# Kernel tuning notes

Measured on AMD Instinct MI355X. Metric: run time of the kernel, lower is better.

Reference implementation:

```python
import jax, jax.numpy as jnp
import numpy as np
from jax import lax

N_FFT = 1024
HOP = 64
SR = 16000
N_MELS = 80
N_ITER = 300
N_FRAMES = 512
N_BINS = N_FFT // 2 + 1  # 513
SIG_LEN = N_FFT + HOP * (N_FRAMES - 1)  # 33728 (center=False istft length)

# periodic hann window (librosa default, sym=False)
_WIN_NP = (0.5 - 0.5 * np.cos(2.0 * np.pi * np.arange(N_FFT) / N_FFT)).astype(np.float32)
_WIN = jnp.asarray(_WIN_NP)
# frame gather indices for center=False framing: [N_FRAMES, N_FFT]
_FRAME_IDX_NP = np.arange(N_FRAMES)[:, None] * HOP + np.arange(N_FFT)[None, :]
_FRAME_IDX = jnp.asarray(_FRAME_IDX_NP)
# window-sum-squares normalization for istft overlap-add
_wss = np.zeros(SIG_LEN, np.float32)
np.add.at(_wss, _FRAME_IDX_NP, np.broadcast_to(_WIN_NP**2, (N_FRAMES, N_FFT)))
_WSS_SAFE = jnp.asarray(np.where(_wss > 1e-11, _wss, 1.0).astype(np.float32))


def _mel_filterbank(sr, n_fft, n_mels, fmin=0.0, fmax=None):
    """librosa.filters.mel with defaults: slaney mel scale, slaney norm."""
    if fmax is None:
        fmax = sr / 2.0
    f_sp = 200.0 / 3.0
    min_log_hz = 1000.0
    min_log_mel = min_log_hz / f_sp
    logstep = np.log(6.4) / 27.0

    def hz2mel(f):
        f = np.asarray(f, dtype=np.float64)
        return np.where(f >= min_log_hz,
                        min_log_mel + np.log(np.maximum(f, min_log_hz) / min_log_hz) / logstep,
                        f / f_sp)

    def mel2hz(m):
        m = np.asarray(m, dtype=np.float64)
        return np.where(m >= min_log_mel,
                        min_log_hz * np.exp(logstep * (m - min_log_mel)),
                        m * f_sp)

    mel_f = mel2hz(np.linspace(hz2mel(fmin), hz2mel(fmax), n_mels + 2))
    fft_f = np.linspace(0.0, sr / 2.0, 1 + n_fft // 2)
    fdiff = np.diff(mel_f)
    ramps = mel_f[:, None] - fft_f[None, :]
    lower = -ramps[:-2] / fdiff[:-1, None]
    upper = ramps[2:] / fdiff[1:, None]
    weights = np.maximum(0.0, np.minimum(lower, upper))
    enorm = 2.0 / (mel_f[2:n_mels + 2] - mel_f[:n_mels])  # slaney norm
    weights *= enorm[:, None]
    return weights.astype(np.float32)  # [n_mels, n_bins]


def _stft(x):
    # x: [SIG_LEN] -> [N_BINS, N_FRAMES], center=False, hann window
    frames = x[_FRAME_IDX] * _WIN  # [N_FRAMES, N_FFT]
    return jnp.fft.rfft(frames, axis=-1).T


def _istft(S):
    # S: [N_BINS, N_FRAMES] -> [SIG_LEN], center=False, hann window, NOLA norm
    frames = jnp.fft.irfft(S.T, n=N_FFT, axis=-1) * _WIN  # [N_FRAMES, N_FFT]
    ola = jnp.zeros(SIG_LEN, dtype=frames.dtype).at[_FRAME_IDX].add(frames)
    return ola / _WSS_SAFE


def setup_inputs() -> dict:
    key = jax.random.key(0)
    mel = jax.random.normal(key, (N_MELS, N_FRAMES), dtype=jnp.float32)
    basis = _mel_filterbank(SR, N_FFT, N_MELS)           # [80, 513]
    inv_mel_basis = np.linalg.pinv(basis).astype(np.float32)  # [513, 80]
    return {"mel": mel, "inv_mel_basis": jnp.asarray(inv_mel_basis)}


def reference(mel, inv_mel_basis):
    # mel -> linear magnitude via pseudo-inverse mel basis
    mag = inv_mel_basis @ jnp.power(10.0, mel)  # [N_BINS, N_FRAMES]

    def step(X_best, _):
        x_t = _istft(X_best)
        est = _stft(x_t)
        phase = est / jnp.maximum(1e-8, jnp.abs(est))
        return (mag * phase).astype(jnp.complex64), None

    X0 = mag.astype(jnp.complex64)
    X_final, _ = lax.scan(step, X0, None, length=N_ITER)
    return jnp.real(_istft(X_final))  # [SIG_LEN]
```

## Files before the change

kernel.cpp:

```cpp
#include <hip/hip_runtime.h>
#include <math.h>

#define NFFT   1024
#define NH     512
#define HOP    64
#define NMELS  80
#define NFR    512
#define NBINS  513
#define NITER  300
#define SIGLEN 33728
#define NSEG   527
#define NT     256
#define NB     512

#define TBL_WIN  0
#define TBL_TWR  1024
#define TBL_TWI  1280
#define TBL_W1R  1536
#define TBL_W1I  2056
#define OFF_MAG  4096
#define OFF_IWS  266752
#define OFF_F    300480
#define OFF_F2   824768
#define FGEN     1349056

typedef unsigned long long u64;
typedef unsigned int u32;

__device__ __forceinline__ float4 coh_load4(const float* p) {
    u64 a = __hip_atomic_load((const u64*)p,       __ATOMIC_RELAXED, __HIP_MEMORY_SCOPE_AGENT);
    u64 b = __hip_atomic_load((const u64*)(p + 2), __ATOMIC_RELAXED, __HIP_MEMORY_SCOPE_AGENT);
    float2 fa, fb;
    __builtin_memcpy(&fa, &a, 8);
    __builtin_memcpy(&fb, &b, 8);
    return make_float4(fa.x, fa.y, fb.x, fb.y);
}
__device__ __forceinline__ void coh_store4(float* p, float4 v) {
    float2 fa = make_float2(v.x, v.y), fb = make_float2(v.z, v.w);
    u64 a, b;
    __builtin_memcpy(&a, &fa, 8);
    __builtin_memcpy(&b, &fb, 8);
    __hip_atomic_store((u64*)p,       a, __ATOMIC_RELAXED, __HIP_MEMORY_SCOPE_AGENT);
    __hip_atomic_store((u64*)(p + 2), b, __ATOMIC_RELAXED, __HIP_MEMORY_SCOPE_AGENT);
}
__device__ __forceinline__ float coh_load1(const float* p) {
    u32 a = __hip_atomic_load((const u32*)p, __ATOMIC_RELAXED, __HIP_MEMORY_SCOPE_AGENT);
    float f;
    __builtin_memcpy(&f, &a, 4);
    return f;
}
__device__ __forceinline__ void flag_store(int* p, int v) {
    __hip_atomic_store(p, v, __ATOMIC_RELAXED, __HIP_MEMORY_SCOPE_AGENT);
}
__device__ __forceinline__ int flag_load(const int* p) {
    return __hip_atomic_load(p, __ATOMIC_RELAXED, __HIP_MEMORY_SCOPE_AGENT);
}
__device__ __forceinline__ float4 f4add(float4 a, float4 b) {
    return make_float4(a.x + b.x, a.y + b.y, a.z + b.z, a.w + b.w);
}

template<int P, int SH, bool INV>
__device__ __forceinline__ void r4b(const float* __restrict__ sR, const float* __restrict__ sI,
                                    float* __restrict__ dR, float* __restrict__ dI,
                                    const float* twr, const float* twi, int j) {
    int k  = j & (P - 1);
    int d0 = ((j - k) << 2) + k;
    float x0r = sR[j],       x0i = sI[j];
    float x1r = sR[j + 128], x1i = sI[j + 128];
    float x2r = sR[j + 256], x2i = sI[j + 256];
    float x3r = sR[j + 384], x3i = sI[j + 384];
    int tb = k << SH;
    float c1 = twr[tb], s1 = twi[tb];
    if (INV) s1 = -s1;
    float c2 = c1 * c1 - s1 * s1, s2 = 2.f * c1 * s1;
    float c3 = c1 * c2 - s1 * s2, s3 = c1 * s2 + s1 * c2;
    float a1r = x1r * c1 - x1i * s1, a1i = x1r * s1 + x1i * c1;
    float a2r = x2r * c2 - x2i * s2, a2i = x2r * s2 + x2i * c2;
    float a3r = x3r * c3 - x3i * s3, a3i = x3r * s3 + x3i * c3;
    float t0r = x0r + a2r, t0i = x0i + a2i;
    float t1r = x0r - a2r, t1i = x0i - a2i;
    float t2r = a1r + a3r, t2i = a1i + a3i;
    float t3r = a1r - a3r, t3i = a1i - a3i;
    float i3r = INV ? -t3i : t3i;
    float i3i = INV ?  t3r : -t3r;
    dR[d0]         = t0r + t2r;  dI[d0]         = t0i + t2i;
    dR[d0 + P]     = t1r + i3r;  dI[d0 + P]     = t1i + i3i;
    dR[d0 + 2 * P] = t0r - t2r;  dI[d0 + 2 * P] = t0i - t2i;
    dR[d0 + 3 * P] = t1r - i3r;  dI[d0 + 3 * P] = t1i - i3i;
}

struct __align__(16) SMemI {
    float xb[NFFT];
    float C0r[NH], C0i[NH];
    float C1r[NH], C1i[NH];
    float win[NFFT];
    float twr[256], twi[256];
    float mag[516];
};

extern "C" __global__ __launch_bounds__(NT)
void k_init(const float* __restrict__ mel,
            const float* __restrict__ invmel,
            float* __restrict__ ws) {
    __shared__ SMemI sm;
    const int tid = threadIdx.x;
    const int t   = blockIdx.x;

    for (int n = tid; n < NFFT; n += NT) {
        double a = (2.0 * 3.14159265358979323846) * (double)n / 1024.0;
        sm.win[n] = (float)(0.5 - 0.5 * cos(a));
    }
    for (int j = tid; j < 256; j += NT) {
        double a = (2.0 * 3.14159265358979323846) * (double)j / 512.0;
        sm.twr[j] = (float)cos(a);
        sm.twi[j] = (float)(-sin(a));
    }
    __syncthreads();
    if (t == 0) {
        for (int n = tid; n < NFFT; n += NT) ws[TBL_WIN + n] = sm.win[n];
        for (int j = tid; j < 256; j += NT) {
            ws[TBL_TWR + j] = sm.twr[j];
            ws[TBL_TWI + j] = sm.twi[j];
        }
        for (int k = tid; k < NBINS; k += NT) {
            double a = (2.0 * 3.14159265358979323846) * (double)k / 1024.0;
            ws[TBL_W1R + k] = (float)cos(a);
            ws[TBL_W1I + k] = (float)sin(a);
        }
        for (int i = tid; i < NFR * 16; i += NT)
            ((int*)ws)[FGEN + i] = 0;
    }

    for (int p = t * NT + tid; p < SIGLEN; p += NFR * NT) {
        int tq = p >> 6, io = p & 63;
        float s = 0.f;
#pragma unroll
        for (int m = 0; m < 16; ++m) {
            int tp = tq - m;
            if (tp >= 0 && tp < NFR) {
                float w = sm.win[io + (m << 6)];
                s += w * w;
            }
        }
        ws[OFF_IWS + p] = (s > 1e-11f) ? (1.0f / s) : 1.0f;
    }

    if (tid < NMELS) sm.xb[tid] = exp10f(mel[tid * NFR + t]);
    __syncthreads();
    for (int k = tid; k < NBINS; k += NT) {
        const float* row = invmel + k * NMELS;
        float s = 0.f;
#pragma unroll 8
        for (int j = 0; j < NMELS; ++j) s += row[j] * sm.xb[j];
        ws[OFF_MAG + t * NBINS + k] = s;
        sm.mag[k] = s;
    }
    __syncthreads();

    for (int k = tid; k < NH; k += NT) {
        float xr = sm.mag[k], yr = sm.mag[512 - k];
        double a = (2.0 * 3.14159265358979323846) * (double)k / 1024.0;
        float c = (float)cos(a), s = (float)sin(a);
        float dr = xr - yr;
        sm.C1r[k] = ((xr + yr) - s * dr) * (1.0f / 1024.0f);
        sm.C1i[k] = (c * dr) * (1.0f / 1024.0f);
    }
    __syncthreads();
    if (tid < 128) {
        float x0r = sm.C1r[tid],       x0i = sm.C1i[tid];
        float x1r = sm.C1r[tid + 128], x1i = sm.C1i[tid + 128];
        float x2r = sm.C1r[tid + 256], x2i = sm.C1i[tid + 256];
        float x3r = sm.C1r[tid + 384], x3i = sm.C1i[tid + 384];
        float t0r = x0r + x2r, t0i = x0i + x2i;
        float t1r = x0r - x2r, t1i = x0i - x2i;
        float t2r = x1r + x3r, t2i = x1i + x3i;
        float t3r = x1r - x3r, t3i = x1i - x3i;
        float4 vr = make_float4(t0r + t2r, t1r - t3i, t0r - t2r, t1r + t3i);
        float4 vi = make_float4(t0i + t2i, t1i + t3r, t0i - t2i, t1i - t3r);
        ((float4*)sm.C0r)[tid] = vr;
        ((float4*)sm.C0i)[tid] = vi;
    }
    __syncthreads();
    if (tid < 128) r4b<4, 5, true>(sm.C0r, sm.C0i, sm.C1r, sm.C1i, sm.twr, sm.twi, tid);
    __syncthreads();
    if (tid < 128) r4b<16, 3, true>(sm.C1r, sm.C1i, sm.C0r, sm.C0i, sm.twr, sm.twi, tid);
    __syncthreads();
    if (tid < 128) r4b<64, 1, true>(sm.C0r, sm.C0i, sm.C1r, sm.C1i, sm.twr, sm.twi, tid);
    __syncthreads();
    {
        float c = sm.twr[tid], s = -sm.twi[tid];
        float x0r = sm.C1r[tid], x0i = sm.C1i[tid];
        float x1r = sm.C1r[tid + 256], x1i = sm.C1i[tid + 256];
        float ar = x1r * c - x1i * s, ai = x1r * s + x1i * c;
        sm.C0r[tid]       = x0r + ar;  sm.C0i[tid]       = x0i + ai;
        sm.C0r[tid + 256] = x0r - ar;  sm.C0i[tid + 256] = x0i - ai;
    }
    __syncthreads();

    float4 w4 = ((float4*)sm.win)[tid];
    float4 o;
    o.x = w4.x * sm.C0r[2 * tid];
    o.y = w4.y * sm.C0i[2 * tid];
    o.z = w4.z * sm.C0r[2 * tid + 1];
    o.w = w4.w * sm.C0i[2 * tid + 1];
    *(float4*)&ws[OFF_F + (t << 10) + (tid << 2)] = o;
}


struct __align__(16) SM1 {
    float C0r[NH], C0i[NH];
    float C1r[NH], C1i[NH];
    float twr[256], twi[256];
};

extern "C" __global__ __launch_bounds__(NT)
void k_persist(float* __restrict__ ws, float* __restrict__ out) {
    __shared__ SM1 sm;
    const int tid = threadIdx.x;
    const int t   = blockIdx.x;
    const int i0  = tid << 2;
    const int j2  = 512 - tid;
    const int n0  = tid << 1;

    const float* tbl  = ws;
    const float* magg = ws + OFF_MAG;
    const float* iws  = ws + OFF_IWS;
    float* F0 = ws + OFF_F;
    float* F1 = ws + OFF_F2;
    int*   fgen = (int*)ws + FGEN;

    if (tid < 64)       ((float4*)sm.twr)[tid]      = ((const float4*)(tbl + TBL_TWR))[tid];
    else if (tid < 128) ((float4*)sm.twi)[tid - 64] = ((const float4*)(tbl + TBL_TWI))[tid - 64];

    float4 w4   = ((const float4*)(tbl + TBL_WIN))[tid];
    float4 iws4 = *(const float4*)&iws[(t << 6) + i0];
    float m_a, m_b, m_ny = 0.f, w1r_a, w1i_a, w1r_b, w1i_b;
    {
        const int s0 = t * NBINS;
        if (tid == 0) {
            m_a = magg[s0]; m_ny = magg[s0 + 512]; m_b = magg[s0 + 256];
            w1r_a = 1.f; w1i_a = 0.f; w1r_b = 0.f; w1i_b = 1.f;
        } else {
            m_a = magg[s0 + tid]; m_b = magg[s0 + j2];
            w1r_a = tbl[TBL_W1R + tid]; w1i_a = tbl[TBL_W1I + tid];
            w1r_b = tbl[TBL_W1R + j2];  w1i_b = tbl[TBL_W1I + j2];
        }
    }
    const bool extra = (t >= 497);
    int gseg = -1;
    if (tid < 64) gseg = t;
    else if (tid < 128 && extra) gseg = t + 15;
    const int u = tid & 63;
    float iwreg = 0.f;
    if (gseg >= 0) iwreg = iws[(gseg << 6) + u];

    const int q    = tid >> 4;
    const int tq   = t + q;
    const int foff = i0 & 63;
    const bool interior = (t >= 15 && t <= NFR - 16);

#pragma unroll 1
    for (int it = 1; it <= NITER; ++it) {
        if (it > 1 && tid < 31) {
            int tp = t - 15 + tid;
            if (tp >= 0 && tp < NFR) {
                const int* fp = fgen + (tp << 4);
                if (flag_load(fp) < it - 1) {
                    do { __builtin_amdgcn_s_sleep(4); } while (flag_load(fp) < it - 1);
                }
            }
        }
        __syncthreads();

        const float* Fs = (it & 1) ? F0 : F1;
        float*       Fd = (it & 1) ? F1 : F0;

        float4 acc;
        if (interior) {
            float4 v0  = coh_load4(&Fs[((tq)      << 10) + foff]);
            float4 v1  = coh_load4(&Fs[((tq - 1)  << 10) + foff + (1 << 6)]);
            float4 v2  = coh_load4(&Fs[((tq - 2)  << 10) + foff + (2 << 6)]);
            float4 v3  = coh_load4(&Fs[((tq - 3)  << 10) + foff + (3 << 6)]);
            float4 v4  = coh_load4(&Fs[((tq - 4)  << 10) + foff + (4 << 6)]);
            float4 v5  = coh_load4(&Fs[((tq - 5)  << 10) + foff + (5 << 6)]);
            float4 v6  = coh_load4(&Fs[((tq - 6)  << 10) + foff + (6 << 6)]);
            float4 v7  = coh_load4(&Fs[((tq - 7)  << 10) + foff + (7 << 6)]);
            float4 v8  = coh_load4(&Fs[((tq - 8)  << 10) + foff + (8 << 6)]);
            float4 v9  = coh_load4(&Fs[((tq - 9)  << 10) + foff + (9 << 6)]);
            float4 v10 = coh_load4(&Fs[((tq - 10) << 10) + foff + (10 << 6)]);
            float4 v11 = coh_load4(&Fs[((tq - 11) << 10) + foff + (11 << 6)]);
            float4 v12 = coh_load4(&Fs[((tq - 12) << 10) + foff + (12 << 6)]);
            float4 v13 = coh_load4(&Fs[((tq - 13) << 10) + foff + (13 << 6)]);
            float4 v14 = coh_load4(&Fs[((tq - 14) << 10) + foff + (14 << 6)]);
            float4 v15 = coh_load4(&Fs[((tq - 15) << 10) + foff + (15 << 6)]);
            float4 s0 = f4add(f4add(v0, v1),  f4add(v2, v3));
            float4 s1 = f4add(f4add(v4, v5),  f4add(v6, v7));
            float4 s2 = f4add(f4add(v8, v9),  f4add(v10, v11));
            float4 s3 = f4add(f4add(v12, v13), f4add(v14, v15));
            acc = f4add(f4add(s0, s1), f4add(s2, s3));
        } else {
            acc = make_float4(0.f, 0.f, 0.f, 0.f);
#pragma unroll
            for (int m = 0; m < 16; ++m) {
                int tp = tq - m;
                if (tp >= 0 && tp < NFR) {
                    float4 x = coh_load4(&Fs[(tp << 10) + foff + (m << 6)]);
                    acc.x += x.x; acc.y += x.y; acc.z += x.z; acc.w += x.w;
                }
            }
        }
        {
            float xx = acc.x * iws4.x;
            float xy = acc.y * iws4.y;
            float xz = acc.z * iws4.z;
            float xw = acc.w * iws4.w;
            sm.C1r[n0]     = xx * w4.x;
            sm.C1i[n0]     = xy * w4.y;
            sm.C1r[n0 + 1] = xz * w4.z;
            sm.C1i[n0 + 1] = xw * w4.w;
        }
        __syncthreads();
        if (tid < 128) {
            float x0r = sm.C1r[tid],       x0i = sm.C1i[tid];
            float x1r = sm.C1r[tid + 128], x1i = sm.C1i[tid + 128];
            float x2r = sm.C1r[tid + 256], x2i = sm.C1i[tid + 256];
            float x3r = sm.C1r[tid + 384], x3i = sm.C1i[tid + 384];
            float t0r = x0r + x2r, t0i = x0i + x2i;
            float t1r = x0r - x2r, t1i = x0i - x2i;
            float t2r = x1r + x3r, t2i = x1i + x3i;
            float t3r = x1r - x3r, t3i = x1i - x3i;
            float4 vr = make_float4(t0r + t2r, t1r + t3i, t0r - t2r, t1r - t3i);
            float4 vi = make_float4(t0i + t2i, t1i - t3r, t0i - t2i, t1i + t3r);
            ((float4*)sm.C0r)[tid] = vr;
            ((float4*)sm.C0i)[tid] = vi;
        }
        __syncthreads();
        if (tid < 128) r4b<4, 5, false>(sm.C0r, sm.C0i, sm.C1r, sm.C1i, sm.twr, sm.twi, tid);
        __syncthreads();
        if (tid < 128) r4b<16, 3, false>(sm.C1r, sm.C1i, sm.C0r, sm.C0i, sm.twr, sm.twi, tid);
        __syncthreads();
        if (tid < 128) r4b<64, 1, false>(sm.C0r, sm.C0i, sm.C1r, sm.C1i, sm.twr, sm.twi, tid);
        __syncthreads();
        {
            float c = sm.twr[tid], s = sm.twi[tid];
            float x0r = sm.C1r[tid], x0i = sm.C1i[tid];
            float x1r = sm.C1r[tid + 256], x1i = sm.C1i[tid + 256];
            float ar = x1r * c - x1i * s, ai = x1r * s + x1i * c;
            sm.C0r[tid]       = x0r + ar;  sm.C0i[tid]       = x0i + ai;
            sm.C0r[tid + 256] = x0r - ar;  sm.C0i[tid + 256] = x0i - ai;
        }
        __syncthreads();

        if (tid == 0) {
            float zr = sm.C0r[0], zi = sm.C0i[0];
            float e0 = zr + zi;
            float e5 = zr - zi;
            float X0 = m_a  * e0 / fmaxf(1e-8f, fabsf(e0));
            float X5 = m_ny * e5 / fmaxf(1e-8f, fabsf(e5));
            sm.C1r[0] = (X0 + X5) * (1.0f / 1024.0f);
            sm.C1i[0] = (X0 - X5) * (1.0f / 1024.0f);
            float z6r = sm.C0r[256], z6i = sm.C0i[256];
            float sc6 = m_b / fmaxf(1e-8f, sqrtf(z6r * z6r + z6i * z6i));
            float X6r = z6r * sc6, X6i = -z6i * sc6;
            sm.C1r[256] = X6r * (2.0f / 1024.0f);
            sm.C1i[256] = -X6i * (2.0f / 1024.0f);
        } else {
            float zr = sm.C0r[tid], zi = sm.C0i[tid];
            float ur = sm.C0r[j2],  ui = sm.C0i[j2];
            float er = 0.5f * (zr + ur), ei = 0.5f * (zi - ui);
            float dr = zr - ur,          di = zi + ui;
            float odr = 0.5f * di, odi = -0.5f * dr;
            float e1r = er + w1r_a * odr + w1i_a * odi;
            float e1i = ei + w1r_a * odi - w1i_a * odr;
            float e2r =  er + w1r_b * odr - w1i_b * odi;
            float e2i = -ei - w1r_b * odi - w1i_b * odr;
            float sc1 = m_a / fmaxf(1e-8f, sqrtf(e1r * e1r + e1i * e1i));
            float sc2 = m_b / fmaxf(1e-8f, sqrtf(e2r * e2r + e2i * e2i));
            float X1r = e1r * sc1, X1i = e1i * sc1;
            float X2r = e2r * sc2, X2i = e2i * sc2;
            float Er = X1r + X2r, Ei = X1i - X2i;
            float Dr = X1r - X2r, Di = X1i + X2i;
            float wdr = w1r_a * Dr - w1i_a * Di, wdi = w1r_a * Di + w1i_a * Dr;
            sm.C1r[tid] = (Er - wdi) * (1.0f / 1024.0f);
            sm.C1i[tid] = (Ei + wdr) * (1.0f / 1024.0f);
            float wdr2 = -w1r_b * Dr - w1i_b * Di, wdi2 = w1r_b * Di - w1i_b * Dr;
            sm.C1r[j2] = (Er - wdi2) * (1.0f / 1024.0f);
            sm.C1i[j2] = (-Ei + wdr2) * (1.0f / 1024.0f);
        }
        __syncthreads();

        if (tid < 128) {
            float x0r = sm.C1r[tid],       x0i = sm.C1i[tid];
            float x1r = sm.C1r[tid + 128], x1i = sm.C1i[tid + 128];
            float x2r = sm.C1r[tid + 256], x2i = sm.C1i[tid + 256];
            float x3r = sm.C1r[tid + 384], x3i = sm.C1i[tid + 384];
            float t0r = x0r + x2r, t0i = x0i + x2i;
            float t1r = x0r - x2r, t1i = x0i - x2i;
            float t2r = x1r + x3r, t2i = x1i + x3i;
            float t3r = x1r - x3r, t3i = x1i - x3i;
            float4 vr = make_float4(t0r + t2r, t1r - t3i, t0r - t2r, t1r + t3i);
            float4 vi = make_float4(t0i + t2i, t1i + t3r, t0i - t2i, t1i - t3r);
            ((float4*)sm.C0r)[tid] = vr;
            ((float4*)sm.C0i)[tid] = vi;
        }
        __syncthreads();
        if (tid < 128) r4b<4, 5, true>(sm.C0r, sm.C0i, sm.C1r, sm.C1i, sm.twr, sm.twi, tid);
        __syncthreads();
        if (tid < 128) r4b<16, 3, true>(sm.C1r, sm.C1i, sm.C0r, sm.C0i, sm.twr, sm.twi, tid);
        __syncthreads();
        if (tid < 128) r4b<64, 1, true>(sm.C0r, sm.C0i, sm.C1r, sm.C1i, sm.twr, sm.twi, tid);
        __syncthreads();
        {
            float c = sm.twr[tid], s = -sm.twi[tid];
            float x0r = sm.C1r[tid], x0i = sm.C1i[tid];
            float x1r = sm.C1r[tid + 256], x1i = sm.C1i[tid + 256];
            float ar = x1r * c - x1i * s, ai = x1r * s + x1i * c;
            sm.C0r[tid]       = x0r + ar;  sm.C0i[tid]       = x0i + ai;
            sm.C0r[tid + 256] = x0r - ar;  sm.C0i[tid + 256] = x0i - ai;
        }
        __syncthreads();

        {
            float4 o;
            o.x = w4.x * sm.C0r[n0];
            o.y = w4.y * sm.C0i[n0];
            o.z = w4.z * sm.C0r[n0 + 1];
            o.w = w4.w * sm.C0i[n0 + 1];
            coh_store4(&Fd[(t << 10) + i0], o);
        }
        __syncthreads();
        if (tid == 0)
            flag_store(fgen + (t << 4), it);
    }

    if (gseg >= 0 && u < 16) {
        int tp = gseg - u;
        if (tp >= 0 && tp < NFR) {
            const int* fp = fgen + (tp << 4);
            if (flag_load(fp) < NITER) {
                do { __builtin_amdgcn_s_sleep(4); } while (flag_load(fp) < NITER);
            }
        }
    }
    __syncthreads();
    if (gseg >= 0) {
        float acc = 0.f;
#pragma unroll
        for (int m = 0; m < 16; ++m) {
            int tp = gseg - m;
            if (tp >= 0 && tp < NFR)
                acc += coh_load1(&F0[(tp << 10) + u + (m << 6)]);
        }
        out[(gseg << 6) + u] = acc * iwreg;
    }
}

extern "C" void kernel_launch(void* const* d_in, const int* in_sizes, int n_in,
                              void* d_out, int out_size, void* d_ws, size_t ws_size,
                              hipStream_t stream) {
    const float* mel    = (const float*)d_in[0];
    const float* invmel = (const float*)d_in[1];
    float* out = (float*)d_out;
    float* ws  = (float*)d_ws;

    k_init<<<NFR, NT, 0, stream>>>(mel, invmel, ws);
    k_persist<<<NB, NT, 0, stream>>>(ws, out);
}
```

Baseline: 2.980 ms.

## Per-thread flag polling, inline-asm dwordx4 coherent IO, fuse final FFT stages

Each thread now polls only the 16 producer flags it actually reads instead of having 31 threads poll and then hit a block barrier, which removes one __syncthreads per iteration. Coherent loads and stores of the frame buffer become single global_load/store_dwordx4 with sc1 via inline asm, replacing pairs of 64-bit atomics. The last radix-2 FFT stage is folded into the real-spectrum post-processing and into the output store, with twiddles preloaded into registers, removing two shared-memory passes and their barriers. This adds redundant flag loads per thread, and relies on raw asm cache bits being correct for cross-block visibility.

```diff
diff --git a/kernel.cpp b/kernel.cpp
--- a/kernel.cpp
+++ b/kernel.cpp
@@ -26,6 +26,7 @@
 
 typedef unsigned long long u64;
 typedef unsigned int u32;
+typedef float f32x4 __attribute__((ext_vector_type(4)));
 
 __device__ __forceinline__ float4 coh_load4(const float* p) {
     u64 a = __hip_atomic_load((const u64*)p,       __ATOMIC_RELAXED, __HIP_MEMORY_SCOPE_AGENT);
@@ -35,14 +36,6 @@
     __builtin_memcpy(&fb, &b, 8);
     return make_float4(fa.x, fa.y, fb.x, fb.y);
 }
-__device__ __forceinline__ void coh_store4(float* p, float4 v) {
-    float2 fa = make_float2(v.x, v.y), fb = make_float2(v.z, v.w);
-    u64 a, b;
-    __builtin_memcpy(&a, &fa, 8);
-    __builtin_memcpy(&b, &fb, 8);
-    __hip_atomic_store((u64*)p,       a, __ATOMIC_RELAXED, __HIP_MEMORY_SCOPE_AGENT);
-    __hip_atomic_store((u64*)(p + 2), b, __ATOMIC_RELAXED, __HIP_MEMORY_SCOPE_AGENT);
-}
 __device__ __forceinline__ float coh_load1(const float* p) {
     u32 a = __hip_atomic_load((const u32*)p, __ATOMIC_RELAXED, __HIP_MEMORY_SCOPE_AGENT);
     float f;
@@ -55,9 +48,15 @@
 __device__ __forceinline__ int flag_load(const int* p) {
     return __hip_atomic_load(p, __ATOMIC_RELAXED, __HIP_MEMORY_SCOPE_AGENT);
 }
-__device__ __forceinline__ float4 f4add(float4 a, float4 b) {
-    return make_float4(a.x + b.x, a.y + b.y, a.z + b.z, a.w + b.w);
-}
+__device__ __forceinline__ f32x4 coh_load4v(const float* p) {
+    f32x4 r;
+    asm volatile("global_load_dwordx4 %0, %1, off sc1" : "=v"(r) : "v"(p) : "memory");
+    return r;
+}
+__device__ __forceinline__ void coh_store4v(float* p, f32x4 v) {
+    asm volatile("global_store_dwordx4 %0, %1, off sc1" :: "v"(p), "v"(v) : "memory");
+}
+__device__ __forceinline__ f32x4 v4add(f32x4 a, f32x4 b) { return a + b; }
 
 template<int P, int SH, bool INV>
 __device__ __forceinline__ void r4b(const float* __restrict__ sR, const float* __restrict__ sI,
@@ -254,6 +253,12 @@
     float iwreg = 0.f;
     if (gseg >= 0) iwreg = iws[(gseg << 6) + u];
 
+    __syncthreads();
+    const float tcp = sm.twr[tid], tsp = sm.twi[tid];
+    const int a0 = (2 * tid) & 255, a1 = (2 * tid + 1) & 255;
+    const float tc0 = sm.twr[a0], ts0 = sm.twi[a0];
+    const float tc1 = sm.twr[a1], ts1 = sm.twi[a1];
+
     const int q    = tid >> 4;
     const int tq   = t + q;
     const int foff = i0 & 63;
@@ -261,59 +266,69 @@
 
 #pragma unroll 1
     for (int it = 1; it <= NITER; ++it) {
-        if (it > 1 && tid < 31) {
-            int tp = t - 15 + tid;
-            if (tp >= 0 && tp < NFR) {
-                const int* fp = fgen + (tp << 4);
-                if (flag_load(fp) < it - 1) {
-                    do { __builtin_amdgcn_s_sleep(4); } while (flag_load(fp) < it - 1);
+        if (it > 1) {
+            const int need = it - 1;
+            for (;;) {
+                int mn = 0x7fffffff;
+#pragma unroll
+                for (int m = 0; m < 16; ++m) {
+                    int tp = tq - m;
+                    if (tp >= 0 && tp < NFR) {
+                        int g = flag_load(fgen + (tp << 4));
+                        mn = (g < mn) ? g : mn;
+                    }
                 }
+                if (mn >= need) break;
+                __builtin_amdgcn_s_sleep(2);
             }
         }
-        __syncthreads();
 
         const float* Fs = (it & 1) ? F0 : F1;
         float*       Fd = (it & 1) ? F1 : F0;
 
-        float4 acc;
+        float accx, accy, accz, accw;
         if (interior) {
-            float4 v0  = coh_load4(&Fs[((tq)      << 10) + foff]);
-            float4 v1  = coh_load4(&Fs[((tq - 1)  << 10) + foff + (1 << 6)]);
-            float4 v2  = coh_load4(&Fs[((tq - 2)  << 10) + foff + (2 << 6)]);
-            float4 v3  = coh_load4(&Fs[((tq - 3)  << 10) + foff + (3 << 6)]);
-            float4 v4  = coh_load4(&Fs[((tq - 4)  << 10) + foff + (4 << 6)]);
-            float4 v5  = coh_load4(&Fs[((tq - 5)  << 10) + foff + (5 << 6)]);
-            float4 v6  = coh_load4(&Fs[((tq - 6)  << 10) + foff + (6 << 6)]);
-            float4 v7  = coh_load4(&Fs[((tq - 7)  << 10) + foff + (7 << 6)]);
-            float4 v8  = coh_load4(&Fs[((tq - 8)  << 10) + foff + (8 << 6)]);
-            float4 v9  = coh_load4(&Fs[((tq - 9)  << 10) + foff + (9 << 6)]);
-            float4 v10 = coh_load4(&Fs[((tq - 10) << 10) + foff + (10 << 6)]);
-            float4 v11 = coh_load4(&Fs[((tq - 11) << 10) + foff + (11 << 6)]);
-            float4 v12 = coh_load4(&Fs[((tq - 12) << 10) + foff + (12 << 6)]);
-            float4 v13 = coh_load4(&Fs[((tq - 13) << 10) + foff + (13 << 6)]);
-            float4 v14 = coh_load4(&Fs[((tq - 14) << 10) + foff + (14 << 6)]);
-            float4 v15 = coh_load4(&Fs[((tq - 15) << 10) + foff + (15 << 6)]);
-            float4 s0 = f4add(f4add(v0, v1),  f4add(v2, v3));
-            float4 s1 = f4add(f4add(v4, v5),  f4add(v6, v7));
-            float4 s2 = f4add(f4add(v8, v9),  f4add(v10, v11));
-            float4 s3 = f4add(f4add(v12, v13), f4add(v14, v15));
-            acc = f4add(f4add(s0, s1), f4add(s2, s3));
+            const float* bp = Fs + (tq << 10) + foff;
+            f32x4 v0  = coh_load4v(bp);
+            f32x4 v1  = coh_load4v(bp - 960);
+            f32x4 v2  = coh_load4v(bp - 1920);
+            f32x4 v3  = coh_load4v(bp - 2880);
+            f32x4 v4  = coh_load4v(bp - 3840);
+            f32x4 v5  = coh_load4v(bp - 4800);
+            f32x4 v6  = coh_load4v(bp - 5760);
+            f32x4 v7  = coh_load4v(bp - 6720);
+            f32x4 v8  = coh_load4v(bp - 7680);
+            f32x4 v9  = coh_load4v(bp - 8640);
+            f32x4 v10 = coh_load4v(bp - 9600);
+            f32x4 v11 = coh_load4v(bp - 10560);
+            f32x4 v12 = coh_load4v(bp - 11520);
+            f32x4 v13 = coh_load4v(bp - 12480);
+            f32x4 v14 = coh_load4v(bp - 13440);
+            f32x4 v15 = coh_load4v(bp - 14400);
+            asm volatile("s_waitcnt vmcnt(0)" ::: "memory");
+            __builtin_amdgcn_sched_barrier(0);
+            f32x4 s0 = (v0 + v1)   + (v2 + v3);
+            f32x4 s1 = (v4 + v5)   + (v6 + v7);
+            f32x4 s2 = (v8 + v9)   + (v10 + v11);
+            f32x4 s3 = (v12 + v13) + (v14 + v15);
+            f32x4 a  = (s0 + s1) + (s2 + s3);
+            accx = a.x; accy = a.y; accz = a.z; accw = a.w;
         } else {
-            acc = make_float4(0.f, 0.f, 0.f, 0.f);
+            accx = 0.f; accy = 0.f; accz = 0.f; accw = 0.f;
 #pragma unroll
             for (int m = 0; m < 16; ++m) {
                 int tp = tq - m;
                 if (tp >= 0 && tp < NFR) {
                     float4 x = coh_load4(&Fs[(tp << 10) + foff + (m << 6)]);
-                    acc.x += x.x; acc.y += x.y; acc.z += x.z; acc.w += x.w;
+                    accx += x.x; accy += x.y; accz += x.z; accw += x.w;
                 }
             }
         }
         {
-            float xx = acc.x * iws4.x;
-            float xy = acc.y * iws4.y;
-            float xz = acc.z * iws4.z;
-            float xw = acc.w * iws4.w;
+            float xx = accx * iws4.x;
+            float xy = accy * iws4.y;
+            float xz = accz * iws4.z;
+            float xw = accw * iws4.w;
             sm.C1r[n0]     = xx * w4.x;
             sm.C1i[n0]     = xy * w4.y;
             sm.C1r[n0 + 1] = xz * w4.z;
@@ -341,32 +356,31 @@
         __syncthreads();
         if (tid < 128) r4b<64, 1, false>(sm.C0r, sm.C0i, sm.C1r, sm.C1i, sm.twr, sm.twi, tid);
         __syncthreads();
-        {
-            float c = sm.twr[tid], s = sm.twi[tid];
-            float x0r = sm.C1r[tid], x0i = sm.C1i[tid];
-            float x1r = sm.C1r[tid + 256], x1i = sm.C1i[tid + 256];
-            float ar = x1r * c - x1i * s, ai = x1r * s + x1i * c;
-            sm.C0r[tid]       = x0r + ar;  sm.C0i[tid]       = x0i + ai;
-            sm.C0r[tid + 256] = x0r - ar;  sm.C0i[tid + 256] = x0i - ai;
-        }
-        __syncthreads();
 
         if (tid == 0) {
-            float zr = sm.C0r[0], zi = sm.C0i[0];
+            float x0r = sm.C1r[0], x0i = sm.C1i[0];
+            float x1r = sm.C1r[256], x1i = sm.C1i[256];
+            float zr = x0r + x1r, zi = x0i + x1i;
+            float z6r = x0r - x1r, z6i = x0i - x1i;
             float e0 = zr + zi;
             float e5 = zr - zi;
             float X0 = m_a  * e0 / fmaxf(1e-8f, fabsf(e0));
             float X5 = m_ny * e5 / fmaxf(1e-8f, fabsf(e5));
-            sm.C1r[0] = (X0 + X5) * (1.0f / 1024.0f);
-            sm.C1i[0] = (X0 - X5) * (1.0f / 1024.0f);
-            float z6r = sm.C0r[256], z6i = sm.C0i[256];
+            sm.C0r[0] = (X0 + X5) * (1.0f / 1024.0f);
+            sm.C0i[0] = (X0 - X5) * (1.0f / 1024.0f);
             float sc6 = m_b / fmaxf(1e-8f, sqrtf(z6r * z6r + z6i * z6i));
             float X6r = z6r * sc6, X6i = -z6i * sc6;
-            sm.C1r[256] = X6r * (2.0f / 1024.0f);
-            sm.C1i[256] = -X6i * (2.0f / 1024.0f);
+            sm.C0r[256] = X6r * (2.0f / 1024.0f);
+            sm.C0i[256] = -X6i * (2.0f / 1024.0f);
         } else {
-            float zr = sm.C0r[tid], zi = sm.C0i[tid];
-            float ur = sm.C0r[j2],  ui = sm.C0i[j2];
+            float x0r = sm.C1r[tid],       x0i = sm.C1i[tid];
+            float x1r = sm.C1r[tid + 256], x1i = sm.C1i[tid + 256];
+            float ar = x1r * tcp - x1i * tsp, ai = x1r * tsp + x1i * tcp;
+            float zr = x0r + ar, zi = x0i + ai;
+            float y0r = sm.C1r[256 - tid], y0i = sm.C1i[256 - tid];
+            float y1r = sm.C1r[512 - tid], y1i = sm.C1i[512 - tid];
+            float br = y1r * (-tcp) - y1i * tsp, bi = y1r * tsp + y1i * (-tcp);
+            float ur = y0r - br, ui = y0i - bi;
             float er = 0.5f * (zr + ur), ei = 0.5f * (zi - ui);
             float dr = zr - ur,          di = zi + ui;
             float odr = 0.5f * di, odi = -0.5f * dr;
@@ -381,52 +395,64 @@
             float Er = X1r + X2r, Ei = X1i - X2i;
             float Dr = X1r - X2r, Di = X1i + X2i;
             float wdr = w1r_a * Dr - w1i_a * Di, wdi = w1r_a * Di + w1i_a * Dr;
-            sm.C1r[tid] = (Er - wdi) * (1.0f / 1024.0f);
-            sm.C1i[tid] = (Ei + wdr) * (1.0f / 1024.0f);
+            sm.C0r[tid] = (Er - wdi) * (1.0f / 1024.0f);
+            sm.C0i[tid] = (Ei + wdr) * (1.0f / 1024.0f);
             float wdr2 = -w1r_b * Dr - w1i_b * Di, wdi2 = w1r_b * Di - w1i_b * Dr;
-            sm.C1r[j2] = (Er - wdi2) * (1.0f / 1024.0f);
-            sm.C1i[j2] = (-Ei + wdr2) * (1.0f / 1024.0f);
+            sm.C0r[j2] = (Er - wdi2) * (1.0f / 1024.0f);
+            sm.C0i[j2] = (-Ei + wdr2) * (1.0f / 1024.0f);
         }
         __syncthreads();
 
         if (tid < 128) {
-            float x0r = sm.C1r[tid],       x0i = sm.C1i[tid];
-            float x1r = sm.C1r[tid + 128], x1i = sm.C1i[tid + 128];
-            float x2r = sm.C1r[tid + 256], x2i = sm.C1i[tid + 256];
-            float x3r = sm.C1r[tid + 384], x3i = sm.C1i[tid + 384];
+            float x0r = sm.C0r[tid],       x0i = sm.C0i[tid];
+            float x1r = sm.C0r[tid + 128], x1i = sm.C0i[tid + 128];
+            float x2r = sm.C0r[tid + 256], x2i = sm.C0i[tid + 256];
+            float x3r = sm.C0r[tid + 384], x3i = sm.C0i[tid + 384];
             float t0r = x0r + x2r, t0i = x0i + x2i;
             float t1r = x0r - x2r, t1i = x0i - x2i;
             float t2r = x1r + x3r, t2i = x1i + x3i;
             float t3r = x1r - x3r, t3i = x1i - x3i;
             float4 vr = make_float4(t0r + t2r, t1r - t3i, t0r - t2r, t1r + t3i);
             float4 vi = make_float4(t0i + t2i, t1i + t3r, t0i - t2i, t1i - t3r);
-            ((float4*)sm.C0r)[tid] = vr;
-            ((float4*)sm.C0i)[tid] = vi;
-        }
-        __syncthreads();
-        if (tid < 128) r4b<4, 5, true>(sm.C0r, sm.C0i, sm.C1r, sm.C1i, sm.twr, sm.twi, tid);
-        __syncthreads();
-        if (tid < 128) r4b<16, 3, true>(sm.C1r, sm.C1i, sm.C0r, sm.C0i, sm.twr, sm.twi, tid);
-        __syncthreads();
-        if (tid < 128) r4b<64, 1, true>(sm.C0r, sm.C0i, sm.C1r, sm.C1i, sm.twr, sm.twi, tid);
-        __syncthreads();
+            ((float4*)sm.C1r)[tid] = vr;
+            ((float4*)sm.C1i)[tid] = vi;
+        }
+        __syncthreads();
+        if (tid < 128) r4b<4, 5, true>(sm.C1r, sm.C1i, sm.C0r, sm.C0i, sm.twr, sm.twi, tid);
+        __syncthreads();
+        if (tid < 128) r4b<16, 3, true>(sm.C0r, sm.C0i, sm.C1r, sm.C1i, sm.twr, sm.twi, tid);
+        __syncthreads();
+        if (tid < 128) r4b<64, 1, true>(sm.C1r, sm.C1i, sm.C0r, sm.C0i, sm.twr, sm.twi, tid);
+        __syncthreads();
+
         {
-            float c = sm.twr[tid], s = -sm.twi[tid];
-            float x0r = sm.C1r[tid], x0i = sm.C1i[tid];
-            float x1r = sm.C1r[tid + 256], x1i = sm.C1i[tid + 256];
-            float ar = x1r * c - x1i * s, ai = x1r * s + x1i * c;
-            sm.C0r[tid]       = x0r + ar;  sm.C0i[tid]       = x0i + ai;
-            sm.C0r[tid + 256] = x0r - ar;  sm.C0i[tid + 256] = x0i - ai;
-        }
-        __syncthreads();
-
-        {
-            float4 o;
-            o.x = w4.x * sm.C0r[n0];
-            o.y = w4.y * sm.C0i[n0];
-            o.z = w4.z * sm.C0r[n0 + 1];
-            o.w = w4.w * sm.C0i[n0 + 1];
-            coh_store4(&Fd[(t << 10) + i0], o);
+            float A0r, A0i, A1r, A1i;
+            const float c0 = tc0, s0 = -ts0, c1 = tc1, s1 = -ts1;
+            if (tid < 128) {
+                float p0r = sm.C0r[n0],       p0i = sm.C0i[n0];
+                float q0r = sm.C0r[n0 + 256], q0i = sm.C0i[n0 + 256];
+                float p1r = sm.C0r[n0 + 1],   p1i = sm.C0i[n0 + 1];
+                float q1r = sm.C0r[n0 + 257], q1i = sm.C0i[n0 + 257];
+                float a0r = q0r * c0 - q0i * s0, a0i = q0r * s0 + q0i * c0;
+                float a1r = q1r * c1 - q1i * s1, a1i = q1r * s1 + q1i * c1;
+                A0r = p0r + a0r; A0i = p0i + a0i;
+                A1r = p1r + a1r; A1i = p1i + a1i;
+            } else {
+                float p0r = sm.C0r[n0 - 256], p0i = sm.C0i[n0 - 256];
+                float q0r = sm.C0r[n0],       q0i = sm.C0i[n0];
+                float p1r = sm.C0r[n0 - 255], p1i = sm.C0i[n0 - 255];
+                float q1r = sm.C0r[n0 + 1],   q1i = sm.C0i[n0 + 1];
+                float a0r = q0r * c0 - q0i * s0, a0i = q0r * s0 + q0i * c0;
+                float a1r = q1r * c1 - q1i * s1, a1i = q1r * s1 + q1i * c1;
+                A0r = p0r - a0r; A0i = p0i - a0i;
+                A1r = p1r - a1r; A1i = p1i - a1i;
+            }
+            f32x4 o;
+            o.x = w4.x * A0r;
+            o.y = w4.y * A0i;
+            o.z = w4.z * A1r;
+            o.w = w4.w * A1i;
+            coh_store4v(&Fd[(t << 10) + i0], o);
         }
         __syncthreads();
         if (tid == 0)
```

Result: slower. 3.647 ms (+22.4%).
